# Kernel tuning notes

Measured on AMD Instinct MI355X. Metric: run time of the kernel, lower is better.

Reference implementation:

```python
import jax, jax.numpy as jnp
import numpy as np

HID, LAT, B, T, E, NB, V = 256, 128, 32, 32, 2048, 10, 6
M = T * E + 1  # message buffer rows; row 0 = zero padding


def _linear_params(key, fan_in, fan_out):
    k1, k2 = jax.random.split(key)
    w = jax.random.normal(k1, (fan_out, fan_in), jnp.float32) * 0.05
    b = jax.random.normal(k2, (fan_out,), jnp.float32) * 0.05
    return w, b


def setup_inputs() -> dict:
    key = jax.random.key(0)
    ks = jax.random.split(key, 20)
    inp = {}
    inp["tree_latent_vec"] = jax.random.normal(ks[0], (B, LAT), jnp.float32)
    inp["nei_idx_h"] = jax.random.randint(ks[1], (T, E, NB), 0, M, jnp.int32)
    inp["nei_idx_o"] = jax.random.randint(ks[2], (T, E, NB), 0, M, jnp.int32)
    inp["cur_labels"] = jax.random.randint(ks[3], (T, E), 0, V, jnp.int32)
    inp["contexts"] = jax.random.randint(ks[4], (T, E), 0, B, jnp.int32)
    inp["direction"] = jax.random.randint(ks[5], (T, E), 0, 2, jnp.int32)
    inp["pred_targets_step"] = jax.random.randint(ks[6], (T, E), 0, V, jnp.int32)
    inp["root_labels"] = jax.random.randint(ks[7], (B,), 0, V, jnp.int32)
    inp["root_nei_idx"] = jax.random.randint(ks[8], (B, NB), 0, M, jnp.int32)
    inp["Wz_w"], inp["Wz_b"] = _linear_params(ks[9], HID + V, HID)
    inp["Wr_w"], inp["Wr_b"] = _linear_params(ks[10], V, HID)
    inp["Ur_w"], inp["Ur_b"] = _linear_params(ks[11], HID, HID)
    inp["Wh_w"], inp["Wh_b"] = _linear_params(ks[12], HID + V, HID)
    inp["W_w"], inp["W_b"] = _linear_params(ks[13], HID + LAT, HID)
    inp["Wo_w"], inp["Wo_b"] = _linear_params(ks[14], HID, V)
    inp["U_w"], inp["U_b"] = _linear_params(ks[15], HID + LAT, HID)
    inp["Uo_w"], inp["Uo_b"] = _linear_params(ks[16], HID, 1)
    inp["Ui_w"], inp["Ui_b"] = _linear_params(ks[17], HID + V, HID)
    return inp


def reference(tree_latent_vec, Wz_w, Wz_b, Wr_w, Wr_b, Ur_w, Ur_b, Wh_w, Wh_b,
              W_w, W_b, Wo_w, Wo_b, U_w, U_b, Uo_w, Uo_b, Ui_w, Ui_b,
              nei_idx_h, nei_idx_o, cur_labels, contexts, direction,
              pred_targets_step, root_labels, root_nei_idx):
    cur_x_all = jax.nn.one_hot(cur_labels, V, dtype=jnp.float32)  # [T,E,V]

    def gru(x, h_nei):  # JTNN tree-GRU: x [E,V], h_nei [E,NB,HID]
        sum_h = h_nei.sum(axis=1)
        z = jax.nn.sigmoid(jnp.concatenate([x, sum_h], -1) @ Wz_w.T + Wz_b)
        r = jax.nn.sigmoid((x @ Wr_w.T + Wr_b)[:, None, :]
                           + h_nei @ Ur_w.T + Ur_b)
        gated = (r * h_nei).sum(axis=1)
        pre_h = jnp.tanh(jnp.concatenate([x, gated], -1) @ Wh_w.T + Wh_b)
        return (1.0 - z) * sum_h + z * pre_h

    def step(H, xs):
        t, nih, nio, x = xs
        h_nei = H[nih]                   # [E,NB,HID] gather
        new_h = gru(x, h_nei)            # [E,HID]
        cur_o = H[nio].sum(axis=1)       # [E,HID]
        write_idx = 1 + t * E + jnp.arange(E, dtype=jnp.int32)
        H = H.at[write_idx].set(new_h)   # scatter new messages
        return H, (new_h, cur_o)

    H0 = jnp.zeros((M, HID), jnp.float32)
    ts = jnp.arange(T, dtype=jnp.int32)
    H_final, (new_h_all, cur_o_all) = jax.lax.scan(
        step, H0, (ts, nei_idx_h, nei_idx_o, cur_x_all))

    # ---- word (pred) head ----
    pred_hid = jnp.concatenate(
        [jnp.zeros((B, HID), jnp.float32), new_h_all.reshape(-1, HID)], 0)
    pred_ctx = jnp.concatenate(
        [jnp.arange(B, dtype=jnp.int32), contexts.reshape(-1)], 0)
    pred_tgt = jnp.concatenate([root_labels, pred_targets_step.reshape(-1)], 0)
    pred_mask = jnp.concatenate(
        [jnp.ones((B,), jnp.float32),
         (direction.reshape(-1) == 1).astype(jnp.float32)], 0)
    inp = jnp.concatenate([pred_hid, tree_latent_vec[pred_ctx]], -1)
    pred_scores = jax.nn.relu(inp @ W_w.T + W_b) @ Wo_w.T + Wo_b  # [N,V]
    logp = jax.nn.log_softmax(pred_scores, axis=-1)
    ce = -jnp.take_along_axis(logp, pred_tgt[:, None], axis=1)[:, 0]
    pred_loss = jnp.sum(ce * pred_mask) / B
    preds = jnp.argmax(pred_scores, axis=1)
    pred_acc = jnp.sum((preds == pred_tgt).astype(jnp.float32) * pred_mask) \
        / jnp.sum(pred_mask)

    # ---- stop head ----
    root_x = jax.nn.one_hot(root_labels, V, dtype=jnp.float32)
    root_o = H_final[root_nei_idx].sum(axis=1)                    # [B,HID]
    stop_hid = jnp.concatenate(
        [jnp.concatenate([cur_x_all, cur_o_all], -1).reshape(-1, V + HID),
         jnp.concatenate([root_x, root_o], -1)], 0)
    stop_ctx = jnp.concatenate(
        [contexts.reshape(-1), jnp.arange(B, dtype=jnp.int32)], 0)
    stop_tgt = jnp.concatenate(
        [direction.reshape(-1).astype(jnp.float32),
         jnp.zeros((B,), jnp.float32)], 0)
    h1 = jax.nn.relu(stop_hid @ Ui_w.T + Ui_b)
    inp2 = jnp.concatenate([h1, tree_latent_vec[stop_ctx]], -1)
    s = (jax.nn.relu(inp2 @ U_w.T + U_b) @ Uo_w.T + Uo_b)[:, 0]
    # BCEWithLogits, reduction='sum'
    stop_loss = jnp.sum(jnp.maximum(s, 0.0) - s * stop_tgt
                        + jnp.log1p(jnp.exp(-jnp.abs(s)))) / B
    stops = (s >= 0).astype(jnp.float32)
    stop_acc = jnp.mean((stops == stop_tgt).astype(jnp.float32))

    return jnp.stack([pred_loss, stop_loss,
                      jax.lax.stop_gradient(pred_acc),
                      jax.lax.stop_gradient(stop_acc)])
```

## Files before the change

### kernel.cpp

```cpp
#include <hip/hip_runtime.h>
#include <math.h>

#define HID 256
#define LAT 128
#define BB  32
#define TT  32
#define EE  2048
#define NBR 10
#define VV  6
#define TE  (TT*EE)
#define NROWS (TE + BB)
#define MROWS (TE + 1)

typedef __attribute__((ext_vector_type(8))) short bfrag;
typedef __attribute__((ext_vector_type(4))) float ffrag;

__device__ __forceinline__ float sigmoidf_(float x) { return 1.0f / (1.0f + expf(-x)); }

__device__ __forceinline__ float bf2f(unsigned short u) {
    union { unsigned int i; float f; } x; x.i = ((unsigned int)u) << 16; return x.f;
}
__device__ __forceinline__ unsigned short f2bf(float f) {
    union { float f; unsigned int i; } x; x.f = f;
    unsigned int r = x.i + 0x7FFFu + ((x.i >> 16) & 1u);
    return (unsigned short)(r >> 16);
}

__global__ __launch_bounds__(256) void prep_all(
    const float* __restrict__ Wz, const float* __restrict__ Wh,
    const float* __restrict__ Ur, const float* __restrict__ Ui,
    const float* __restrict__ Ww, const float* __restrict__ Uw,
    unsigned short* __restrict__ dWz, unsigned short* __restrict__ dWh,
    unsigned short* __restrict__ dUr, unsigned short* __restrict__ dUi,
    unsigned short* __restrict__ dWw, unsigned short* __restrict__ dUw)
{
    const int n = blockIdx.x, k = threadIdx.x;
    const float* s; unsigned short* d; int ldw, koff;
    switch (blockIdx.y) {
        case 0:  s = Wz; d = dWz; ldw = 262; koff = VV; break;
        case 1:  s = Wh; d = dWh; ldw = 262; koff = VV; break;
        case 2:  s = Ur; d = dUr; ldw = 256; koff = 0;  break;
        case 3:  s = Ui; d = dUi; ldw = 262; koff = VV; break;
        case 4:  s = Ww; d = dWw; ldw = 384; koff = 0;  break;
        default: s = Uw; d = dUw; ldw = 384; koff = 0;  break;
    }
    d[n * 256 + k] = f2bf(s[(size_t)n * ldw + koff + k]);
}

__global__ __launch_bounds__(256) void prep_cols(
    const float* __restrict__ Wz_w, const float* __restrict__ Wz_b,
    const float* __restrict__ Wh_w, const float* __restrict__ Wh_b,
    const float* __restrict__ Wr_w, const float* __restrict__ Wr_b,
    const float* __restrict__ Ur_b,
    const float* __restrict__ Ui_w, const float* __restrict__ Ui_b,
    float* __restrict__ zcol, float* __restrict__ hcol,
    float* __restrict__ rcol, float* __restrict__ icol)
{
    const int v = blockIdx.x, h = threadIdx.x;
    zcol[v * 256 + h] = Wz_w[h * 262 + v] + Wz_b[h];
    hcol[v * 256 + h] = Wh_w[h * 262 + v] + Wh_b[h];
    rcol[v * 256 + h] = Wr_w[h * VV + v] + Wr_b[h] + Ur_b[h];
    icol[v * 256 + h] = Ui_w[h * 262 + v] + Ui_b[h];
}

__global__ __launch_bounds__(256) void lat_gemm2(
    const float* __restrict__ lat,
    const float* __restrict__ W0, const float* __restrict__ W1,
    float* __restrict__ out0, float* __restrict__ out1)
{
    const int b = blockIdx.x, h = threadIdx.x;
    const float* W = blockIdx.y ? W1 : W0;
    float* out     = blockIdx.y ? out1 : out0;
    float acc = 0.f;
    #pragma unroll 4
    for (int k = 0; k < LAT; ++k)
        acc += lat[b * LAT + k] * W[h * 384 + 256 + k];
    out[b * 256 + h] = acc;
}

#define SFP 268
#define SHP 280

__global__ __launch_bounds__(256) void step_fused(
    const unsigned short* __restrict__ Hb,
    const unsigned short* __restrict__ Ub,
    const int* __restrict__ nih, const int* __restrict__ nio,
    const int* __restrict__ labels,
    const float* __restrict__ rcol, const float* __restrict__ zcol,
    const float* __restrict__ hcol,
    const unsigned short* __restrict__ Wzb,
    const unsigned short* __restrict__ Whb,
    const unsigned short* __restrict__ Urb,
    unsigned short* __restrict__ HbW, unsigned short* __restrict__ UbW,
    unsigned short* __restrict__ curOb,
    int rowg_base)
{
    __shared__ float          s_sum[16][SFP];
    __shared__ unsigned short s_gat[16][SHP];
    __shared__ unsigned short s_nh [16][SHP];
    __shared__ int s_idxh[8][NBR];
    __shared__ int s_idxo[8][NBR];
    __shared__ int s_lbl[16];

    const int tid = threadIdx.x;
    const int e0  = blockIdx.x * 8;

    if (tid < 80) {
        s_idxh[tid / NBR][tid % NBR] = nih[e0 * NBR + tid];
    } else if (tid < 160) {
        const int t = tid - 80;
        s_idxo[t / NBR][t % NBR] = nio[e0 * NBR + t];
    } else if (tid < 176) {
        const int t = tid - 160;
        s_lbl[t] = (t < 8) ? labels[e0 + t] : 0;
    }
    {
        const int zr = 8 + (tid >> 5), zd = (tid & 31) * 8;
        *reinterpret_cast<float4*>(&s_sum[zr][zd])     = make_float4(0.f, 0.f, 0.f, 0.f);
        *reinterpret_cast<float4*>(&s_sum[zr][zd + 4]) = make_float4(0.f, 0.f, 0.f, 0.f);
        const uint4 z4 = make_uint4(0u, 0u, 0u, 0u);
        *reinterpret_cast<uint4*>(&s_gat[zr][zd]) = z4;
        *reinterpret_cast<uint4*>(&s_nh [zr][zd]) = z4;
    }
    __syncthreads();

    const int w = tid >> 6;
    const int l = tid & 63;

    {
        const int el = tid >> 5;
        const int h0 = (tid & 31) * 8;
        float s[8], g[8], o[8], rc[8];
        #pragma unroll
        for (int j = 0; j < 8; ++j) { s[j] = 0.f; g[j] = 0.f; o[j] = 0.f; }
        const int lb = s_lbl[el];
        #pragma unroll
        for (int j = 0; j < 8; ++j) rc[j] = rcol[lb * 256 + h0 + j];

        #pragma unroll
        for (int nb = 0; nb < NBR; ++nb) {
            const int ih = s_idxh[el][nb];
            if ((unsigned)(ih - rowg_base) >= (unsigned)EE) {
                uint4 hv = *reinterpret_cast<const uint4*>(Hb + (size_t)ih * 256 + h0);
                uint4 uv = *reinterpret_cast<const uint4*>(Ub + (size_t)ih * 256 + h0);
                const unsigned short* hp = reinterpret_cast<const unsigned short*>(&hv);
                const unsigned short* up = reinterpret_cast<const unsigned short*>(&uv);
                #pragma unroll
                for (int j = 0; j < 8; ++j) {
                    const float hf = bf2f(hp[j]);
                    s[j] += hf;
                    g[j] += hf * sigmoidf_(rc[j] + bf2f(up[j]));
                }
            }
            const int io = s_idxo[el][nb];
            if ((unsigned)(io - rowg_base) >= (unsigned)EE) {
                uint4 ov = *reinterpret_cast<const uint4*>(Hb + (size_t)io * 256 + h0);
                const unsigned short* op = reinterpret_cast<const unsigned short*>(&ov);
                #pragma unroll
                for (int j = 0; j < 8; ++j) o[j] += bf2f(op[j]);
            }
        }
        *reinterpret_cast<float4*>(&s_sum[el][h0])     = make_float4(s[0], s[1], s[2], s[3]);
        *reinterpret_cast<float4*>(&s_sum[el][h0 + 4]) = make_float4(s[4], s[5], s[6], s[7]);
        union { unsigned short u[8]; uint4 v; } gu, ou;
        #pragma unroll
        for (int j = 0; j < 8; ++j) { gu.u[j] = f2bf(g[j]); ou.u[j] = f2bf(o[j]); }
        *reinterpret_cast<uint4*>(&s_gat[el][h0]) = gu.v;
        *reinterpret_cast<uint4*>(curOb + (size_t)(e0 + el) * 256 + h0) = ou.v;
    }
    __syncthreads();

    const int ar  = l & 15;
    const int kg  = (l >> 4) * 8;
    const int nb0 = w * 64;

    ffrag zacc[4], pacc[4];
    #pragma unroll
    for (int nt = 0; nt < 4; ++nt) {
        zacc[nt] = (ffrag){0.f, 0.f, 0.f, 0.f};
        pacc[nt] = (ffrag){0.f, 0.f, 0.f, 0.f};
    }
    #pragma unroll
    for (int ks = 0; ks < 8; ++ks) {
        const int k0 = ks * 32 + kg;
        bfrag az;
        const float* ap = &s_sum[ar][k0];
        #pragma unroll
        for (int j = 0; j < 8; ++j) az[j] = (short)f2bf(ap[j]);
        bfrag ah = *reinterpret_cast<const bfrag*>(&s_gat[ar][k0]);
        #pragma unroll
        for (int nt = 0; nt < 4; ++nt) {
            const int n = nb0 + nt * 16 + ar;
            bfrag bz = *reinterpret_cast<const bfrag*>(Wzb + (size_t)n * 256 + k0);
            bfrag bh = *reinterpret_cast<const bfrag*>(Whb + (size_t)n * 256 + k0);
            zacc[nt] = __builtin_amdgcn_mfma_f32_16x16x32_bf16(az, bz, zacc[nt], 0, 0, 0);
            pacc[nt] = __builtin_amdgcn_mfma_f32_16x16x32_bf16(ah, bh, pacc[nt], 0, 0, 0);
        }
    }

    #pragma unroll
    for (int nt = 0; nt < 4; ++nt) {
        const int n = nb0 + nt * 16 + (l & 15);
        #pragma unroll
        for (int r = 0; r < 4; ++r) {
            const int m = (l >> 4) * 4 + r;
            if (m < 8) {
                const int lb = s_lbl[m];
                const float z  = sigmoidf_(zacc[nt][r] + zcol[lb * 256 + n]);
                const float ph = tanhf(pacc[nt][r] + hcol[lb * 256 + n]);
                const float nh = (1.f - z) * s_sum[m][n] + z * ph;
                s_nh[m][n] = f2bf(nh);
            }
        }
    }
    __syncthreads();

    {
        const int row = tid >> 5, c8 = (tid & 31) * 8;
        uint4 v = *reinterpret_cast<const uint4*>(&s_nh[row][c8]);
        *reinterpret_cast<uint4*>(HbW + (size_t)(rowg_base + e0 + row) * 256 + c8) = v;
    }

    ffrag uacc[4];
    #pragma unroll
    for (int nt = 0; nt < 4; ++nt) uacc[nt] = (ffrag){0.f, 0.f, 0.f, 0.f};
    #pragma unroll
    for (int ks = 0; ks < 8; ++ks) {
        const int k0 = ks * 32 + kg;
        bfrag a = *reinterpret_cast<const bfrag*>(&s_nh[ar][k0]);
        #pragma unroll
        for (int nt = 0; nt < 4; ++nt) {
            const int n = nb0 + nt * 16 + ar;
            bfrag b = *reinterpret_cast<const bfrag*>(Urb + (size_t)n * 256 + k0);
            uacc[nt] = __builtin_amdgcn_mfma_f32_16x16x32_bf16(a, b, uacc[nt], 0, 0, 0);
        }
    }
    #pragma unroll
    for (int nt = 0; nt < 4; ++nt) {
        const int n = nb0 + nt * 16 + (l & 15);
        #pragma unroll
        for (int r = 0; r < 4; ++r) {
            const int m = (l >> 4) * 4 + r;
            if (m < 8) s_gat[m][n] = f2bf(uacc[nt][r]);
        }
    }
    __syncthreads();
    {
        const int row = tid >> 5, c8 = (tid & 31) * 8;
        uint4 v = *reinterpret_cast<const uint4*>(&s_gat[row][c8]);
        *reinterpret_cast<uint4*>(UbW + (size_t)(rowg_base + e0 + row) * 256 + c8) = v;
    }
}

template<int EPI>
__global__ __launch_bounds__(256) void hgemm(
    const unsigned short* __restrict__ A, int M,
    const unsigned short* __restrict__ Wb,
    const int* __restrict__ lab1, const int* __restrict__ lab2,
    const float* __restrict__ icol,
    unsigned short* __restrict__ C)
{
    __shared__ unsigned short sbuf[64 * 264];
    __shared__ int s_lb[64];

    const int tid = threadIdx.x;
    const int m0  = blockIdx.x * 64;

    if (EPI == 1 && tid < 64) {
        const int r = m0 + tid;
        int lb = 0;
        if (r < M) lb = (r < TE) ? lab1[r] : lab2[r - TE];
        s_lb[tid] = lb;
    }

    const int w  = tid >> 6;
    const int l  = tid & 63;
    const int ar = l & 15;
    const int kg = (l >> 4) * 8;
    const int lrow = tid >> 2;
    const int lcol = (tid & 3) * 8;

    ffrag acc[4][4];
    #pragma unroll
    for (int mt = 0; mt < 4; ++mt)
        #pragma unroll
        for (int nt = 0; nt < 4; ++nt)
            acc[mt][nt] = (ffrag){0.f, 0.f, 0.f, 0.f};

    for (int kc = 0; kc < 8; ++kc) {
        const int k0 = kc * 32;
        uint4 av = make_uint4(0u, 0u, 0u, 0u);
        if (m0 + lrow < M)
            av = *reinterpret_cast<const uint4*>(A + (size_t)(m0 + lrow) * 256 + k0 + lcol);
        if (kc) __syncthreads();
        *reinterpret_cast<uint4*>(&sbuf[lrow * 40 + lcol]) = av;
        __syncthreads();
        bfrag a[4];
        #pragma unroll
        for (int mt = 0; mt < 4; ++mt)
            a[mt] = *reinterpret_cast<const bfrag*>(&sbuf[(mt * 16 + ar) * 40 + kg]);
        #pragma unroll
        for (int nt = 0; nt < 4; ++nt) {
            const int n = w * 64 + nt * 16 + ar;
            bfrag b = *reinterpret_cast<const bfrag*>(Wb + (size_t)n * 256 + k0 + kg);
            #pragma unroll
            for (int mt = 0; mt < 4; ++mt)
                acc[mt][nt] = __builtin_amdgcn_mfma_f32_16x16x32_bf16(a[mt], b, acc[mt][nt], 0, 0, 0);
        }
    }
    __syncthreads();

    #pragma unroll
    for (int mt = 0; mt < 4; ++mt) {
        #pragma unroll
        for (int nt = 0; nt < 4; ++nt) {
            const int n = w * 64 + nt * 16 + (l & 15);
            #pragma unroll
            for (int r = 0; r < 4; ++r) {
                const int m = mt * 16 + (l >> 4) * 4 + r;
                float v = acc[mt][nt][r];
                if (EPI == 1) v = fmaxf(v + icol[s_lb[m] * 256 + n], 0.f);
                sbuf[m * 264 + n] = f2bf(v);
            }
        }
    }
    __syncthreads();
    {
        const int row = tid >> 2;
        const int cb  = (tid & 3) * 64;
        if (m0 + row < M) {
            #pragma unroll
            for (int q = 0; q < 8; ++q) {
                const int col = cb + q * 8;
                uint4 v = *reinterpret_cast<const uint4*>(&sbuf[row * 264 + col]);
                *reinterpret_cast<uint4*>(C + (size_t)(m0 + row) * 256 + col) = v;
            }
        }
    }
}

__global__ __launch_bounds__(256) void root_o_kernel(
    const unsigned short* __restrict__ Hb, const int* __restrict__ rni,
    unsigned short* __restrict__ dst)
{
    const int b = blockIdx.x, h = threadIdx.x;
    float o = 0.f;
    #pragma unroll
    for (int nb = 0; nb < NBR; ++nb)
        o += bf2f(Hb[(size_t)rni[b * NBR + nb] * 256 + h]);
    dst[(size_t)b * 256 + h] = f2bf(o);
}

__global__ __launch_bounds__(64) void pred_head(
    const unsigned short* __restrict__ pre, const float* __restrict__ latW,
    const float* __restrict__ W_b,
    const float* __restrict__ Wo_w, const float* __restrict__ Wo_b,
    const int* __restrict__ contexts, const int* __restrict__ direction,
    const int* __restrict__ ptgt, const int* __restrict__ root_labels,
    float* __restrict__ part)
{
    __shared__ unsigned short sv[64][264];
    const int l  = threadIdx.x;
    const int r0 = blockIdx.x * 64;

    for (int it = 0; it < 32; ++it) {
        const int rr  = it * 2 + (l >> 5);
        const int row = r0 + rr;
        const int d0  = (l & 31) * 8;
        float v[8];
        if (row < NROWS) {
            const int c = (row < TE) ? contexts[row] : (row - TE);
            uint4 pv = make_uint4(0u, 0u, 0u, 0u);
            if (row < TE)
                pv = *reinterpret_cast<const uint4*>(pre + (size_t)row * 256 + d0);
            const unsigned short* pp = reinterpret_cast<const unsigned short*>(&pv);
            const float4 la = *reinterpret_cast<const float4*>(latW + c * 256 + d0);
            const float4 lb = *reinterpret_cast<const float4*>(latW + c * 256 + d0 + 4);
            const float4 ba = *reinterpret_cast<const float4*>(W_b + d0);
            const float4 bb = *reinterpret_cast<const float4*>(W_b + d0 + 4);
            const float lv[8] = {la.x, la.y, la.z, la.w, lb.x, lb.y, lb.z, lb.w};
            const float bv[8] = {ba.x, ba.y, ba.z, ba.w, bb.x, bb.y, bb.z, bb.w};
            #pragma unroll
            for (int j = 0; j < 8; ++j) {
                float x = lv[j] + bv[j];
                if (row < TE) x += bf2f(pp[j]);
                v[j] = fmaxf(x, 0.f);
            }
        } else {
            #pragma unroll
            for (int j = 0; j < 8; ++j) v[j] = 0.f;
        }
        union { unsigned short u[8]; uint4 q; } uu;
        #pragma unroll
        for (int j = 0; j < 8; ++j) uu.u[j] = f2bf(v[j]);
        *reinterpret_cast<uint4*>(&sv[rr][d0]) = uu.q;
    }
    __syncthreads();

    const int row = r0 + l;
    if (row >= NROWS) return;
    float sc[VV];
    #pragma unroll
    for (int c = 0; c < VV; ++c) sc[c] = Wo_b[c];
    for (int it = 0; it < 32; ++it) {
        const int d0 = it * 8;
        bfrag vv = *reinterpret_cast<const bfrag*>(&sv[l][d0]);
        #pragma unroll
        for (int j = 0; j < 8; ++j) {
            const float x = bf2f((unsigned short)vv[j]);
            #pragma unroll
            for (int c = 0; c < VV; ++c)
                sc[c] += x * Wo_w[c * 256 + d0 + j];
        }
    }
    int tgt; float mask;
    if (row < TE) {
        tgt  = ptgt[row];
        mask = (direction[row] == 1) ? 1.f : 0.f;
    } else {
        tgt  = root_labels[row - TE];
        mask = 1.f;
    }
    float mx = sc[0]; int am = 0;
    #pragma unroll
    for (int c = 1; c < VV; ++c)
        if (sc[c] > mx) { mx = sc[c]; am = c; }
    float se = 0.f;
    #pragma unroll
    for (int c = 0; c < VV; ++c) se += expf(sc[c] - mx);
    const float lse = mx + logf(se);
    const float ce = lse - sc[tgt];
    part[(size_t)row * 3 + 0] = ce * mask;
    part[(size_t)row * 3 + 1] = mask;
    part[(size_t)row * 3 + 2] = (am == tgt) ? mask : 0.f;
}

__global__ __launch_bounds__(64) void stop_head(
    const unsigned short* __restrict__ pre2, const float* __restrict__ latW2,
    const float* __restrict__ U_b,
    const float* __restrict__ Uo_w, const float* __restrict__ Uo_b,
    const int* __restrict__ contexts, const int* __restrict__ direction,
    float* __restrict__ part2)
{
    __shared__ unsigned short sv[64][264];
    const int l  = threadIdx.x;
    const int r0 = blockIdx.x * 64;

    for (int it = 0; it < 32; ++it) {
        const int rr  = it * 2 + (l >> 5);
        const int row = r0 + rr;
        const int d0  = (l & 31) * 8;
        float v[8];
        if (row < NROWS) {
            const int c = (row < TE) ? contexts[row] : (row - TE);
            uint4 pv = *reinterpret_cast<const uint4*>(pre2 + (size_t)row * 256 + d0);
            const unsigned short* pp = reinterpret_cast<const unsigned short*>(&pv);
            const float4 la = *reinterpret_cast<const float4*>(latW2 + c * 256 + d0);
            const float4 lb = *reinterpret_cast<const float4*>(latW2 + c * 256 + d0 + 4);
            const float4 ba = *reinterpret_cast<const float4*>(U_b + d0);
            const float4 bb = *reinterpret_cast<const float4*>(U_b + d0 + 4);
            const float lv[8] = {la.x, la.y, la.z, la.w, lb.x, lb.y, lb.z, lb.w};
            const float bv[8] = {ba.x, ba.y, ba.z, ba.w, bb.x, bb.y, bb.z, bb.w};
            #pragma unroll
            for (int j = 0; j < 8; ++j)
                v[j] = fmaxf(bf2f(pp[j]) + lv[j] + bv[j], 0.f);
        } else {
            #pragma unroll
            for (int j = 0; j < 8; ++j) v[j] = 0.f;
        }
        union { unsigned short u[8]; uint4 q; } uu;
        #pragma unroll
        for (int j = 0; j < 8; ++j) uu.u[j] = f2bf(v[j]);
        *reinterpret_cast<uint4*>(&sv[rr][d0]) = uu.q;
    }
    __syncthreads();

    const int row = r0 + l;
    if (row >= NROWS) return;
    float s = Uo_b[0];
    for (int it = 0; it < 32; ++it) {
        const int d0 = it * 8;
        bfrag vv = *reinterpret_cast<const bfrag*>(&sv[l][d0]);
        #pragma unroll
        for (int j = 0; j < 8; ++j)
            s += bf2f((unsigned short)vv[j]) * Uo_w[d0 + j];
    }
    const float tgt = (row < TE) ? (float)direction[row] : 0.f;
    const float loss = fmaxf(s, 0.f) - s * tgt + log1pf(expf(-fabsf(s)));
    const float stop = (s >= 0.f) ? 1.f : 0.f;
    part2[(size_t)row * 2 + 0] = loss;
    part2[(size_t)row * 2 + 1] = (stop == tgt) ? 1.f : 0.f;
}

__global__ __launch_bounds__(256) void reduce_parts(
    const float* __restrict__ p1, const float* __restrict__ p2,
    float* __restrict__ accum)
{
    float a[5] = {0.f, 0.f, 0.f, 0.f, 0.f};
    const int stride = gridDim.x * blockDim.x;
    for (int r = blockIdx.x * blockDim.x + threadIdx.x; r < NROWS; r += stride) {
        a[0] += p1[(size_t)r * 3 + 0];
        a[1] += p1[(size_t)r * 3 + 1];
        a[2] += p1[(size_t)r * 3 + 2];
        a[3] += p2[(size_t)r * 2 + 0];
        a[4] += p2[(size_t)r * 2 + 1];
    }
    __shared__ float red[5][4];
    const int lane = threadIdx.x & 63, wv = threadIdx.x >> 6;
    #pragma unroll
    for (int i = 0; i < 5; ++i) {
        float x = a[i];
        #pragma unroll
        for (int off = 32; off; off >>= 1) x += __shfl_down(x, off);
        if (lane == 0) red[i][wv] = x;
    }
    __syncthreads();
    if (threadIdx.x < 5) {
        const float s = red[threadIdx.x][0] + red[threadIdx.x][1] +
                        red[threadIdx.x][2] + red[threadIdx.x][3];
        atomicAdd(&accum[threadIdx.x], s);
    }
}

__global__ void finalize(const float* __restrict__ accum, float* __restrict__ out)
{
    if (threadIdx.x == 0) {
        out[0] = accum[0] / (float)BB;
        out[1] = accum[3] / (float)BB;
        out[2] = accum[2] / accum[1];
        out[3] = accum[4] / (float)NROWS;
    }
}

extern "C" void kernel_launch(void* const* d_in, const int* in_sizes, int n_in,
                              void* d_out, int out_size, void* d_ws, size_t ws_size,
                              hipStream_t stream)
{
    const float* lat  = (const float*)d_in[0];
    const int*   nih  = (const int*)d_in[1];
    const int*   nio  = (const int*)d_in[2];
    const int*   lbl  = (const int*)d_in[3];
    const int*   ctx  = (const int*)d_in[4];
    const int*   dir  = (const int*)d_in[5];
    const int*   ptg  = (const int*)d_in[6];
    const int*   rlb  = (const int*)d_in[7];
    const int*   rni  = (const int*)d_in[8];
    const float* Wz_w = (const float*)d_in[9],  *Wz_b = (const float*)d_in[10];
    const float* Wr_w = (const float*)d_in[11], *Wr_b = (const float*)d_in[12];
    const float* Ur_w = (const float*)d_in[13], *Ur_b = (const float*)d_in[14];
    const float* Wh_w = (const float*)d_in[15], *Wh_b = (const float*)d_in[16];
    const float* W_w  = (const float*)d_in[17], *W_b  = (const float*)d_in[18];
    const float* Wo_w = (const float*)d_in[19], *Wo_b = (const float*)d_in[20];
    const float* U_w  = (const float*)d_in[21], *U_b  = (const float*)d_in[22];
    const float* Uo_w = (const float*)d_in[23], *Uo_b = (const float*)d_in[24];
    const float* Ui_w = (const float*)d_in[25], *Ui_b = (const float*)d_in[26];

    char* p = (char*)d_ws;
    auto alloc = [&](size_t bytes) -> void* {
        void* r = (void*)p; p += (bytes + 255) & ~(size_t)255; return r;
    };
    const size_t RB2 = (size_t)NROWS * 256 * sizeof(unsigned short);
    unsigned short* Hb    = (unsigned short*)alloc(RB2);
    unsigned short* Ub    = (unsigned short*)alloc(RB2);
    unsigned short* curOb = (unsigned short*)alloc(RB2);
    unsigned short* h1b   = (unsigned short*)alloc(RB2);
    unsigned short* pre2b = (unsigned short*)alloc(RB2);
    unsigned short* Wzb = (unsigned short*)alloc(65536 * 2);
    unsigned short* Whb = (unsigned short*)alloc(65536 * 2);
    unsigned short* Urb = (unsigned short*)alloc(65536 * 2);
    unsigned short* Uib = (unsigned short*)alloc(65536 * 2);
    unsigned short* Wwb = (unsigned short*)alloc(65536 * 2);
    unsigned short* Uwb = (unsigned short*)alloc(65536 * 2);
    float* zcol  = (float*)alloc(VV * 256 * 4);
    float* hcol  = (float*)alloc(VV * 256 * 4);
    float* rcol  = (float*)alloc(VV * 256 * 4);
    float* icol  = (float*)alloc(VV * 256 * 4);
    float* latW  = (float*)alloc(BB * 256 * 4);
    float* latW2 = (float*)alloc(BB * 256 * 4);
    float* part1 = (float*)alloc((size_t)NROWS * 3 * 4);
    float* part2 = (float*)alloc((size_t)NROWS * 2 * 4);
    float* accum = (float*)alloc(32);

    hipMemsetAsync(Hb, 0, RB2, stream);
    hipMemsetAsync(Ub, 0, RB2, stream);
    hipMemsetAsync(accum, 0, 32, stream);

    prep_all<<<dim3(256, 6), 256, 0, stream>>>(Wz_w, Wh_w, Ur_w, Ui_w, W_w, U_w,
                                               Wzb, Whb, Urb, Uib, Wwb, Uwb);
    prep_cols<<<VV, 256, 0, stream>>>(Wz_w, Wz_b, Wh_w, Wh_b, Wr_w, Wr_b, Ur_b,
                                      Ui_w, Ui_b, zcol, hcol, rcol, icol);
    lat_gemm2<<<dim3(BB, 2), 256, 0, stream>>>(lat, W_w, U_w, latW, latW2);

    for (int t = 0; t < TT; ++t) {
        step_fused<<<EE / 8, 256, 0, stream>>>(
            Hb, Ub, nih + (size_t)t * EE * NBR, nio + (size_t)t * EE * NBR,
            lbl + t * EE, rcol, zcol, hcol, Wzb, Whb, Urb,
            Hb, Ub, curOb + (size_t)t * EE * 256, 1 + t * EE);
    }

    root_o_kernel<<<BB, 256, 0, stream>>>(Hb, rni, curOb + (size_t)TE * 256);

    hgemm<1><<<(NROWS + 63) / 64, 256, 0, stream>>>(curOb, NROWS, Uib, lbl, rlb, icol, h1b);
    hgemm<0><<<(NROWS + 63) / 64, 256, 0, stream>>>(h1b, NROWS, Uwb, nullptr, nullptr, nullptr, pre2b);
    stop_head<<<(NROWS + 63) / 64, 64, 0, stream>>>(pre2b, latW2, U_b, Uo_w, Uo_b, ctx, dir, part2);

    hgemm<0><<<TE / 64, 256, 0, stream>>>(Hb + 256, TE, Wwb, nullptr, nullptr, nullptr, h1b);
    pred_head<<<(NROWS + 63) / 64, 64, 0, stream>>>(h1b, latW, W_b, Wo_w, Wo_b,
                                                    ctx, dir, ptg, rlb, part1);

    reduce_parts<<<256, 256, 0, stream>>>(part1, part2, accum);
    finalize<<<1, 64, 0, stream>>>(accum, (float*)d_out);
}
```

Baseline: 1.316 ms.

## Replace per-step kernel launches with one cooperative persistent kernel using grid sync

The 32 sequential step_fused launches become a single cooperative kernel that loops over time steps and separates them with grid.sync. Each block now runs 512 threads (8 waves), each wave doing half the output columns, and the gather work is split into 4-wide chunks. The aim is to remove per-launch overhead and tail effects between dependent steps. In exchange it adds grid-wide barrier cost and needs all 256 blocks to be co-resident, with the higher thread count putting pressure on registers.

```diff
diff --git a/kernel.cpp b/kernel.cpp
--- a/kernel.cpp
+++ b/kernel.cpp
@@ -1,5 +1,8 @@
 #include <hip/hip_runtime.h>
+#include <hip/hip_cooperative_groups.h>
 #include <math.h>
+
+namespace cg = cooperative_groups;
 
 #define HID 256
 #define LAT 128
@@ -81,40 +84,34 @@
 #define SFP 268
 #define SHP 280
 
-__global__ __launch_bounds__(256) void step_fused(
-    const unsigned short* __restrict__ Hb,
-    const unsigned short* __restrict__ Ub,
-    const int* __restrict__ nih, const int* __restrict__ nio,
-    const int* __restrict__ labels,
+__global__ __launch_bounds__(512) void scan_coop(
+    unsigned short* __restrict__ Hb,
+    unsigned short* __restrict__ Ub,
+    const int* __restrict__ nih_all,
+    const int* __restrict__ nio_all,
+    const int* __restrict__ lbl_all,
     const float* __restrict__ rcol, const float* __restrict__ zcol,
     const float* __restrict__ hcol,
     const unsigned short* __restrict__ Wzb,
     const unsigned short* __restrict__ Whb,
     const unsigned short* __restrict__ Urb,
-    unsigned short* __restrict__ HbW, unsigned short* __restrict__ UbW,
-    unsigned short* __restrict__ curOb,
-    int rowg_base)
-{
+    unsigned short* __restrict__ curOb_all)
+{
+    cg::grid_group grid = cg::this_grid();
+
     __shared__ float          s_sum[16][SFP];
     __shared__ unsigned short s_gat[16][SHP];
     __shared__ unsigned short s_nh [16][SHP];
     __shared__ int s_idxh[8][NBR];
     __shared__ int s_idxo[8][NBR];
-    __shared__ int s_lbl[16];
+    __shared__ int s_lbl[8];
 
     const int tid = threadIdx.x;
     const int e0  = blockIdx.x * 8;
-
-    if (tid < 80) {
-        s_idxh[tid / NBR][tid % NBR] = nih[e0 * NBR + tid];
-    } else if (tid < 160) {
-        const int t = tid - 80;
-        s_idxo[t / NBR][t % NBR] = nio[e0 * NBR + t];
-    } else if (tid < 176) {
-        const int t = tid - 160;
-        s_lbl[t] = (t < 8) ? labels[e0 + t] : 0;
-    }
-    {
+    const int w   = tid >> 6;
+    const int l   = tid & 63;
+
+    if (tid < 256) {
         const int zr = 8 + (tid >> 5), zd = (tid & 31) * 8;
         *reinterpret_cast<float4*>(&s_sum[zr][zd])     = make_float4(0.f, 0.f, 0.f, 0.f);
         *reinterpret_cast<float4*>(&s_sum[zr][zd + 4]) = make_float4(0.f, 0.f, 0.f, 0.f);
@@ -122,133 +119,151 @@
         *reinterpret_cast<uint4*>(&s_gat[zr][zd]) = z4;
         *reinterpret_cast<uint4*>(&s_nh [zr][zd]) = z4;
     }
-    __syncthreads();
-
-    const int w = tid >> 6;
-    const int l = tid & 63;
-
-    {
-        const int el = tid >> 5;
-        const int h0 = (tid & 31) * 8;
-        float s[8], g[8], o[8], rc[8];
-        #pragma unroll
-        for (int j = 0; j < 8; ++j) { s[j] = 0.f; g[j] = 0.f; o[j] = 0.f; }
-        const int lb = s_lbl[el];
-        #pragma unroll
-        for (int j = 0; j < 8; ++j) rc[j] = rcol[lb * 256 + h0 + j];
-
-        #pragma unroll
-        for (int nb = 0; nb < NBR; ++nb) {
-            const int ih = s_idxh[el][nb];
-            if ((unsigned)(ih - rowg_base) >= (unsigned)EE) {
-                uint4 hv = *reinterpret_cast<const uint4*>(Hb + (size_t)ih * 256 + h0);
-                uint4 uv = *reinterpret_cast<const uint4*>(Ub + (size_t)ih * 256 + h0);
-                const unsigned short* hp = reinterpret_cast<const unsigned short*>(&hv);
-                const unsigned short* up = reinterpret_cast<const unsigned short*>(&uv);
-                #pragma unroll
-                for (int j = 0; j < 8; ++j) {
-                    const float hf = bf2f(hp[j]);
-                    s[j] += hf;
-                    g[j] += hf * sigmoidf_(rc[j] + bf2f(up[j]));
+
+    for (int t = 0; t < TT; ++t) {
+        const int rowg_base = 1 + t * EE;
+        const int* nih    = nih_all + (size_t)t * EE * NBR;
+        const int* nio    = nio_all + (size_t)t * EE * NBR;
+        const int* labels = lbl_all + t * EE;
+        unsigned short* curOb = curOb_all + (size_t)t * EE * 256;
+
+        if (tid < 80) {
+            s_idxh[tid / NBR][tid % NBR] = nih[e0 * NBR + tid];
+        } else if (tid < 160) {
+            const int q = tid - 80;
+            s_idxo[q / NBR][q % NBR] = nio[e0 * NBR + q];
+        } else if (tid < 168) {
+            s_lbl[tid - 160] = labels[e0 + tid - 160];
+        }
+        __syncthreads();
+
+        {
+            const int el = w;
+            const int h0 = l * 4;
+            float s[4], g[4], o[4], rc[4];
+            #pragma unroll
+            for (int j = 0; j < 4; ++j) { s[j] = 0.f; g[j] = 0.f; o[j] = 0.f; }
+            const int lb = s_lbl[el];
+            const float4 rcv = *reinterpret_cast<const float4*>(rcol + lb * 256 + h0);
+            rc[0] = rcv.x; rc[1] = rcv.y; rc[2] = rcv.z; rc[3] = rcv.w;
+
+            #pragma unroll
+            for (int nb = 0; nb < NBR; ++nb) {
+                const int ih = s_idxh[el][nb];
+                if ((unsigned)(ih - rowg_base) >= (unsigned)EE) {
+                    uint2 hv = *reinterpret_cast<const uint2*>(Hb + (size_t)ih * 256 + h0);
+                    uint2 uv = *reinterpret_cast<const uint2*>(Ub + (size_t)ih * 256 + h0);
+                    const unsigned short* hp = reinterpret_cast<const unsigned short*>(&hv);
+                    const unsigned short* up = reinterpret_cast<const unsigned short*>(&uv);
+                    #pragma unroll
+                    for (int j = 0; j < 4; ++j) {
+                        const float hf = bf2f(hp[j]);
+                        s[j] += hf;
+                        g[j] += hf * sigmoidf_(rc[j] + bf2f(up[j]));
+                    }
                 }
-            }
-            const int io = s_idxo[el][nb];
-            if ((unsigned)(io - rowg_base) >= (unsigned)EE) {
-                uint4 ov = *reinterpret_cast<const uint4*>(Hb + (size_t)io * 256 + h0);
-                const unsigned short* op = reinterpret_cast<const unsigned short*>(&ov);
-                #pragma unroll
-                for (int j = 0; j < 8; ++j) o[j] += bf2f(op[j]);
-            }
-        }
-        *reinterpret_cast<float4*>(&s_sum[el][h0])     = make_float4(s[0], s[1], s[2], s[3]);
-        *reinterpret_cast<float4*>(&s_sum[el][h0 + 4]) = make_float4(s[4], s[5], s[6], s[7]);
-        union { unsigned short u[8]; uint4 v; } gu, ou;
-        #pragma unroll
-        for (int j = 0; j < 8; ++j) { gu.u[j] = f2bf(g[j]); ou.u[j] = f2bf(o[j]); }
-        *reinterpret_cast<uint4*>(&s_gat[el][h0]) = gu.v;
-        *reinterpret_cast<uint4*>(curOb + (size_t)(e0 + el) * 256 + h0) = ou.v;
-    }
-    __syncthreads();
-
-    const int ar  = l & 15;
-    const int kg  = (l >> 4) * 8;
-    const int nb0 = w * 64;
-
-    ffrag zacc[4], pacc[4];
-    #pragma unroll
-    for (int nt = 0; nt < 4; ++nt) {
-        zacc[nt] = (ffrag){0.f, 0.f, 0.f, 0.f};
-        pacc[nt] = (ffrag){0.f, 0.f, 0.f, 0.f};
-    }
-    #pragma unroll
-    for (int ks = 0; ks < 8; ++ks) {
-        const int k0 = ks * 32 + kg;
-        bfrag az;
-        const float* ap = &s_sum[ar][k0];
-        #pragma unroll
-        for (int j = 0; j < 8; ++j) az[j] = (short)f2bf(ap[j]);
-        bfrag ah = *reinterpret_cast<const bfrag*>(&s_gat[ar][k0]);
-        #pragma unroll
-        for (int nt = 0; nt < 4; ++nt) {
-            const int n = nb0 + nt * 16 + ar;
-            bfrag bz = *reinterpret_cast<const bfrag*>(Wzb + (size_t)n * 256 + k0);
-            bfrag bh = *reinterpret_cast<const bfrag*>(Whb + (size_t)n * 256 + k0);
-            zacc[nt] = __builtin_amdgcn_mfma_f32_16x16x32_bf16(az, bz, zacc[nt], 0, 0, 0);
-            pacc[nt] = __builtin_amdgcn_mfma_f32_16x16x32_bf16(ah, bh, pacc[nt], 0, 0, 0);
-        }
-    }
-
-    #pragma unroll
-    for (int nt = 0; nt < 4; ++nt) {
-        const int n = nb0 + nt * 16 + (l & 15);
-        #pragma unroll
-        for (int r = 0; r < 4; ++r) {
-            const int m = (l >> 4) * 4 + r;
-            if (m < 8) {
-                const int lb = s_lbl[m];
-                const float z  = sigmoidf_(zacc[nt][r] + zcol[lb * 256 + n]);
-                const float ph = tanhf(pacc[nt][r] + hcol[lb * 256 + n]);
-                const float nh = (1.f - z) * s_sum[m][n] + z * ph;
-                s_nh[m][n] = f2bf(nh);
-            }
-        }
-    }
-    __syncthreads();
-
-    {
-        const int row = tid >> 5, c8 = (tid & 31) * 8;
-        uint4 v = *reinterpret_cast<const uint4*>(&s_nh[row][c8]);
-        *reinterpret_cast<uint4*>(HbW + (size_t)(rowg_base + e0 + row) * 256 + c8) = v;
-    }
-
-    ffrag uacc[4];
-    #pragma unroll
-    for (int nt = 0; nt < 4; ++nt) uacc[nt] = (ffrag){0.f, 0.f, 0.f, 0.f};
-    #pragma unroll
-    for (int ks = 0; ks < 8; ++ks) {
-        const int k0 = ks * 32 + kg;
-        bfrag a = *reinterpret_cast<const bfrag*>(&s_nh[ar][k0]);
-        #pragma unroll
-        for (int nt = 0; nt < 4; ++nt) {
-            const int n = nb0 + nt * 16 + ar;
-            bfrag b = *reinterpret_cast<const bfrag*>(Urb + (size_t)n * 256 + k0);
-            uacc[nt] = __builtin_amdgcn_mfma_f32_16x16x32_bf16(a, b, uacc[nt], 0, 0, 0);
-        }
-    }
-    #pragma unroll
-    for (int nt = 0; nt < 4; ++nt) {
-        const int n = nb0 + nt * 16 + (l & 15);
-        #pragma unroll
-        for (int r = 0; r < 4; ++r) {
-            const int m = (l >> 4) * 4 + r;
-            if (m < 8) s_gat[m][n] = f2bf(uacc[nt][r]);
-        }
-    }
-    __syncthreads();
-    {
-        const int row = tid >> 5, c8 = (tid & 31) * 8;
-        uint4 v = *reinterpret_cast<const uint4*>(&s_gat[row][c8]);
-        *reinterpret_cast<uint4*>(UbW + (size_t)(rowg_base + e0 + row) * 256 + c8) = v;
+                const int io = s_idxo[el][nb];
+                if ((unsigned)(io - rowg_base) >= (unsigned)EE) {
+                    uint2 ov = *reinterpret_cast<const uint2*>(Hb + (size_t)io * 256 + h0);
+                    const unsigned short* op = reinterpret_cast<const unsigned short*>(&ov);
+                    #pragma unroll
+                    for (int j = 0; j < 4; ++j) o[j] += bf2f(op[j]);
+                }
+            }
+            *reinterpret_cast<float4*>(&s_sum[el][h0]) = make_float4(s[0], s[1], s[2], s[3]);
+            union { unsigned short u[4]; uint2 v; } gu, ou;
+            #pragma unroll
+            for (int j = 0; j < 4; ++j) { gu.u[j] = f2bf(g[j]); ou.u[j] = f2bf(o[j]); }
+            *reinterpret_cast<uint2*>(&s_gat[el][h0]) = gu.v;
+            *reinterpret_cast<uint2*>(curOb + (size_t)(e0 + el) * 256 + h0) = ou.v;
+        }
+        __syncthreads();
+
+        const int ar  = l & 15;
+        const int kg  = (l >> 4) * 8;
+        const int nb0 = w * 32;
+
+        ffrag zacc[2], pacc[2];
+        #pragma unroll
+        for (int nt = 0; nt < 2; ++nt) {
+            zacc[nt] = (ffrag){0.f, 0.f, 0.f, 0.f};
+            pacc[nt] = (ffrag){0.f, 0.f, 0.f, 0.f};
+        }
+        #pragma unroll
+        for (int ks = 0; ks < 8; ++ks) {
+            const int k0 = ks * 32 + kg;
+            bfrag az;
+            const float* ap = &s_sum[ar][k0];
+            #pragma unroll
+            for (int j = 0; j < 8; ++j) az[j] = (short)f2bf(ap[j]);
+            bfrag ah = *reinterpret_cast<const bfrag*>(&s_gat[ar][k0]);
+            #pragma unroll
+            for (int nt = 0; nt < 2; ++nt) {
+                const int n = nb0 + nt * 16 + ar;
+                bfrag bz = *reinterpret_cast<const bfrag*>(Wzb + (size_t)n * 256 + k0);
+                bfrag bh = *reinterpret_cast<const bfrag*>(Whb + (size_t)n * 256 + k0);
+                zacc[nt] = __builtin_amdgcn_mfma_f32_16x16x32_bf16(az, bz, zacc[nt], 0, 0, 0);
+                pacc[nt] = __builtin_amdgcn_mfma_f32_16x16x32_bf16(ah, bh, pacc[nt], 0, 0, 0);
+            }
+        }
+
+        #pragma unroll
+        for (int nt = 0; nt < 2; ++nt) {
+            const int n = nb0 + nt * 16 + (l & 15);
+            #pragma unroll
+            for (int r = 0; r < 4; ++r) {
+                const int m = (l >> 4) * 4 + r;
+                if (m < 8) {
+                    const int lb = s_lbl[m];
+                    const float z  = sigmoidf_(zacc[nt][r] + zcol[lb * 256 + n]);
+                    const float ph = tanhf(pacc[nt][r] + hcol[lb * 256 + n]);
+                    const float nh = (1.f - z) * s_sum[m][n] + z * ph;
+                    s_nh[m][n] = f2bf(nh);
+                }
+            }
+        }
+        __syncthreads();
+
+        {
+            const int row = tid >> 6, c4 = (tid & 63) * 4;
+            uint2 v = *reinterpret_cast<const uint2*>(&s_nh[row][c4]);
+            *reinterpret_cast<uint2*>(Hb + (size_t)(rowg_base + e0 + row) * 256 + c4) = v;
+        }
+
+        ffrag uacc[2];
+        #pragma unroll
+        for (int nt = 0; nt < 2; ++nt) uacc[nt] = (ffrag){0.f, 0.f, 0.f, 0.f};
+        #pragma unroll
+        for (int ks = 0; ks < 8; ++ks) {
+            const int k0 = ks * 32 + kg;
+            bfrag a = *reinterpret_cast<const bfrag*>(&s_nh[ar][k0]);
+            #pragma unroll
+            for (int nt = 0; nt < 2; ++nt) {
+                const int n = nb0 + nt * 16 + ar;
+                bfrag b = *reinterpret_cast<const bfrag*>(Urb + (size_t)n * 256 + k0);
+                uacc[nt] = __builtin_amdgcn_mfma_f32_16x16x32_bf16(a, b, uacc[nt], 0, 0, 0);
+            }
+        }
+        #pragma unroll
+        for (int nt = 0; nt < 2; ++nt) {
+            const int n = nb0 + nt * 16 + (l & 15);
+            #pragma unroll
+            for (int r = 0; r < 4; ++r) {
+                const int m = (l >> 4) * 4 + r;
+                if (m < 8) s_gat[m][n] = f2bf(uacc[nt][r]);
+            }
+        }
+        __syncthreads();
+        {
+            const int row = tid >> 6, c4 = (tid & 63) * 4;
+            uint2 v = *reinterpret_cast<const uint2*>(&s_gat[row][c4]);
+            *reinterpret_cast<uint2*>(Ub + (size_t)(rowg_base + e0 + row) * 256 + c4) = v;
+        }
+
+        if (t + 1 < TT) {
+            __threadfence();
+            grid.sync();
+        }
     }
 }
 
@@ -591,11 +606,14 @@
                                       Ui_w, Ui_b, zcol, hcol, rcol, icol);
     lat_gemm2<<<dim3(BB, 2), 256, 0, stream>>>(lat, W_w, U_w, latW, latW2);
 
-    for (int t = 0; t < TT; ++t) {
-        step_fused<<<EE / 8, 256, 0, stream>>>(
-            Hb, Ub, nih + (size_t)t * EE * NBR, nio + (size_t)t * EE * NBR,
-            lbl + t * EE, rcol, zcol, hcol, Wzb, Whb, Urb,
-            Hb, Ub, curOb + (size_t)t * EE * 256, 1 + t * EE);
+    {
+        void* ka[] = {
+            (void*)&Hb, (void*)&Ub, (void*)&nih, (void*)&nio, (void*)&lbl,
+            (void*)&rcol, (void*)&zcol, (void*)&hcol,
+            (void*)&Wzb, (void*)&Whb, (void*)&Urb, (void*)&curOb
+        };
+        hipLaunchCooperativeKernel((void*)scan_coop, dim3(EE / 8), dim3(512),
+                                   ka, 0, stream);
     }
 
     root_o_kernel<<<BB, 256, 0, stream>>>(Hb, rni, curOb + (size_t)TE * 256);
```

New measurement: 3.051 ms. +131.7%, slower.
